# Kernel optimization log

Measured on AMD Instinct MI355X. Metric: run time of the kernel, lower is better.

Reference implementation:

```python
import jax, jax.numpy as jnp
import numpy as np

EPS = 1e-12  # matches torch F.normalize eps


def _l2_normalize(x):
    n = jnp.linalg.norm(x, axis=-1, keepdims=True)
    return x / jnp.maximum(n, EPS)


def setup_inputs() -> dict:
    key = jax.random.key(0)
    k1, k2, k3 = jax.random.split(key, 3)
    N, E, D = 100000, 1200000, 64
    feat = jax.random.normal(k1, (N, D), dtype=jnp.float32)
    beta = jnp.ones((1,), dtype=jnp.float32)
    src = jax.random.randint(k2, (E,), 0, N, dtype=jnp.int32)
    dst = jax.random.randint(k3, (E,), 0, N, dtype=jnp.int32)
    return {"feat": feat, "beta": beta, "src": src, "dst": dst}


def reference(feat, beta, src, dst):
    N = feat.shape[0]
    # cosine similarity on each edge (AGNN att_type)
    nh = _l2_normalize(feat)                                  # [N, D]
    e = beta[0] * jnp.sum(nh[src] * nh[dst], axis=-1)         # [E]
    # edge softmax over incoming edges of each destination node
    emax = jax.ops.segment_max(e, dst, num_segments=N)        # [N]
    emax = jnp.where(jnp.isfinite(emax), emax, 0.0)           # isolated nodes
    p = jnp.exp(e - emax[dst])                                # [E]
    psum = jax.ops.segment_sum(p, dst, num_segments=N)        # [N]
    p = p / jnp.maximum(psum[dst], EPS)                       # [E]
    # weighted scatter-sum aggregation: h_i' = sum_j p_ij * h_j
    msg = feat[src] * p[:, None]                              # [E, D]
    out = jax.ops.segment_sum(msg, dst, num_segments=N)       # [N, D]
    return out
```

## Files before the change

kernel.cpp:

```cpp
#include <hip/hip_runtime.h>
#include <hip/hip_fp16.h>

#define D 64
#define EPS 1e-12f
#define NPB 512
#define NPB_SHIFT 9
#define NB 256
#define CAP 8192
#define CAP_SHIFT 13
#define EPB 8192
#define SRC_BITS 17

typedef _Float16 hv2 __attribute__((ext_vector_type(2)));

__device__ inline unsigned bc_u(__half2 h) { return __builtin_bit_cast(unsigned, h); }
__device__ inline __half2  bc_h(unsigned u) { return __builtin_bit_cast(__half2, u); }

__device__ inline float fdot2f(unsigned a, unsigned b, float c) {
#if defined(__has_builtin) && __has_builtin(__builtin_amdgcn_fdot2)
    return __builtin_amdgcn_fdot2(__builtin_bit_cast(hv2, a),
                                  __builtin_bit_cast(hv2, b), c, false);
#else
    __half2 ah = bc_h(a), bh = bc_h(b);
    return c + __low2float(ah) * __low2float(bh)
             + __high2float(ah) * __high2float(bh);
#endif
}

__global__ __launch_bounds__(1024) void prep_scatter_kernel(
        const float4* __restrict__ feat4,
        float* __restrict__ norms,
        uint2* __restrict__ nh2,
        const int* __restrict__ src,
        const int* __restrict__ dst,
        int* __restrict__ bincursor,
        unsigned* __restrict__ pairs,
        int N, int E, int BI) {
    __shared__ int hist[NB], offs[NB], cursor[NB], gbase[NB], tmp[NB];
    __shared__ unsigned buf[EPB];
    __shared__ unsigned char binof[EPB];

    if ((int)blockIdx.x < BI) {
        int gid = blockIdx.x * 1024 + threadIdx.x;
        int row = gid >> 4;
        int lg  = gid & 15;
        if (row >= N) return;
        float4 v = feat4[row * 16 + lg];
        float ss = v.x * v.x + v.y * v.y + v.z * v.z + v.w * v.w;
        #pragma unroll
        for (int off = 1; off < 16; off <<= 1) ss += __shfl_xor(ss, off, 64);
        float nrm = fmaxf(sqrtf(ss), EPS);
        float inv = 1.0f / nrm;
        if (lg == 0) norms[row] = nrm;
        uint2 p;
        p.x = bc_u(__floats2half2_rn(v.x * inv, v.y * inv));
        p.y = bc_u(__floats2half2_rn(v.z * inv, v.w * inv));
        nh2[row * 16 + lg] = p;
        return;
    }

    int tid  = threadIdx.x;
    int base = (blockIdx.x - BI) * EPB;
    int cnt  = min(EPB, E - base);

    if (tid < NB) hist[tid] = 0;
    __syncthreads();
    for (int i = tid; i < cnt; i += 1024)
        atomicAdd(&hist[dst[base + i] >> NPB_SHIFT], 1);
    __syncthreads();
    int v = 0;
    if (tid < NB) { v = hist[tid]; tmp[tid] = v; }
    __syncthreads();
    #pragma unroll
    for (int off = 1; off < NB; off <<= 1) {
        int t = 0;
        if (tid < NB && tid >= off) t = tmp[tid - off];
        __syncthreads();
        if (tid < NB) tmp[tid] += t;
        __syncthreads();
    }
    if (tid < NB) {
        int e = tmp[tid] - v;
        offs[tid] = e; cursor[tid] = e;
        if (v > 0)
            gbase[tid] = (tid << CAP_SHIFT) + atomicAdd(&bincursor[tid], v);
    }
    __syncthreads();
    for (int i = tid; i < cnt; i += 1024) {
        int s = src[base + i], dd = dst[base + i];
        int b = dd >> NPB_SHIFT;
        int l = atomicAdd(&cursor[b], 1);
        buf[l]   = ((unsigned)(dd & (NPB - 1)) << SRC_BITS) | (unsigned)s;
        binof[l] = (unsigned char)b;
    }
    __syncthreads();
    for (int i = tid; i < cnt; i += 1024) {
        int b = binof[i];
        pairs[gbase[b] + (i - offs[b])] = buf[i];
    }
}

__global__ __launch_bounds__(1024) void csr_kernel(const unsigned* __restrict__ pairs,
                                                   const int* __restrict__ bincursor,
                                                   int* __restrict__ rowbeg,
                                                   int* __restrict__ rowend,
                                                   int* __restrict__ esrc, int N) {
    __shared__ unsigned buf[CAP];
    __shared__ int hist[NPB], cursor[NPB], tmp[NPB];
    int b    = blockIdx.x;
    int tid  = threadIdx.x;
    int base = b << CAP_SHIFT;
    int cnt  = bincursor[b];
    int node0 = b << NPB_SHIFT;

    if (tid < NPB) hist[tid] = 0;
    __syncthreads();
    for (int i = tid; i < cnt; i += 1024) {
        unsigned p = pairs[base + i];
        buf[i] = p;
        atomicAdd(&hist[p >> SRC_BITS], 1);
    }
    __syncthreads();
    int v = 0;
    if (tid < NPB) { v = hist[tid]; tmp[tid] = v; }
    __syncthreads();
    #pragma unroll
    for (int off = 1; off < NPB; off <<= 1) {
        int t = 0;
        if (tid < NPB && tid >= off) t = tmp[tid - off];
        __syncthreads();
        if (tid < NPB) tmp[tid] += t;
        __syncthreads();
    }
    if (tid < NPB) {
        int excl = tmp[tid] - v;
        cursor[tid] = excl;
        int node = node0 + tid;
        if (node < N) { rowbeg[node] = base + excl; rowend[node] = base + excl + v; }
    }
    __syncthreads();
    for (int i = tid; i < cnt; i += 1024) {
        unsigned p = buf[i];
        int pos = atomicAdd(&cursor[p >> SRC_BITS], 1);
        esrc[base + pos] = (int)(p & ((1u << SRC_BITS) - 1));
    }
}

__global__ __launch_bounds__(256) void gather_kernel(const uint4* __restrict__ nh4,
                                                     const float* __restrict__ norms,
                                                     const float* __restrict__ beta_p,
                                                     const int* __restrict__ rowbeg,
                                                     const int* __restrict__ rowend,
                                                     const int* __restrict__ esrc,
                                                     float4* __restrict__ out4, int N) {
    int gid  = blockIdx.x * blockDim.x + threadIdx.x;
    int d    = gid >> 6;
    int lane = threadIdx.x & 63;
    int g    = lane >> 3;
    int lg   = lane & 7;
    if (d >= N) return;

    int start = rowbeg[d];
    int end   = rowend[d];
    float beta = beta_p[0];

    uint4 fdp = nh4[(size_t)d * 8 + lg];

    __half2 acc0 = __float2half2_rn(0.f), acc1 = acc0, acc2 = acc0, acc3 = acc0;
    float ps = 0.f;

    for (int j0 = start; j0 < end; j0 += 16) {
        int  ja = j0 + g;
        int  jb = ja + 8;
        bool va = (ja < end), vb = (jb < end);
        int  sa = va ? esrc[ja] : 0;
        int  sb = vb ? esrc[jb] : 0;
        uint4 pa = nh4[(size_t)sa * 8 + lg];
        uint4 pb = nh4[(size_t)sb * 8 + lg];
        float nsa = norms[sa], nsb = norms[sb];
        float dpa = fdot2f(pa.x, fdp.x, 0.f);
        float dpb = fdot2f(pb.x, fdp.x, 0.f);
        dpa = fdot2f(pa.y, fdp.y, dpa);  dpb = fdot2f(pb.y, fdp.y, dpb);
        dpa = fdot2f(pa.z, fdp.z, dpa);  dpb = fdot2f(pb.z, fdp.z, dpb);
        dpa = fdot2f(pa.w, fdp.w, dpa);  dpb = fdot2f(pb.w, fdp.w, dpb);
        #pragma unroll
        for (int off = 1; off < 8; off <<= 1) {
            dpa += __shfl_xor(dpa, off, 64);
            dpb += __shfl_xor(dpb, off, 64);
        }
        float wa = va ? __expf(beta * dpa) : 0.f;
        float wb = vb ? __expf(beta * dpb) : 0.f;
        __half2 wa2 = __float2half2_rn(wa * nsa);
        __half2 wb2 = __float2half2_rn(wb * nsb);
        acc0 = __hfma2(wa2, bc_h(pa.x), acc0); acc0 = __hfma2(wb2, bc_h(pb.x), acc0);
        acc1 = __hfma2(wa2, bc_h(pa.y), acc1); acc1 = __hfma2(wb2, bc_h(pb.y), acc1);
        acc2 = __hfma2(wa2, bc_h(pa.z), acc2); acc2 = __hfma2(wb2, bc_h(pb.z), acc2);
        acc3 = __hfma2(wa2, bc_h(pa.w), acc3); acc3 = __hfma2(wb2, bc_h(pb.w), acc3);
        ps += wa + wb;
    }

    #pragma unroll
    for (int off = 8; off < 64; off <<= 1) {
        acc0 = __hadd2(acc0, bc_h(__shfl_xor(bc_u(acc0), off, 64)));
        acc1 = __hadd2(acc1, bc_h(__shfl_xor(bc_u(acc1), off, 64)));
        acc2 = __hadd2(acc2, bc_h(__shfl_xor(bc_u(acc2), off, 64)));
        acc3 = __hadd2(acc3, bc_h(__shfl_xor(bc_u(acc3), off, 64)));
        ps  += __shfl_xor(ps, off, 64);
    }

    if (g == 0) {
        float r = 1.0f / fmaxf(ps, EPS);
        float4 o0 = {__low2float(acc0) * r, __high2float(acc0) * r,
                     __low2float(acc1) * r, __high2float(acc1) * r};
        float4 o1 = {__low2float(acc2) * r, __high2float(acc2) * r,
                     __low2float(acc3) * r, __high2float(acc3) * r};
        out4[(size_t)d * 16 + lg * 2]     = o0;
        out4[(size_t)d * 16 + lg * 2 + 1] = o1;
    }
}

extern "C" void kernel_launch(void* const* d_in, const int* in_sizes, int n_in,
                              void* d_out, int out_size, void* d_ws, size_t ws_size,
                              hipStream_t stream) {
    const float* feat = (const float*)d_in[0];
    const float* beta = (const float*)d_in[1];
    const int*   src  = (const int*)d_in[2];
    const int*   dst  = (const int*)d_in[3];

    int N = in_sizes[0] / D;
    int E = in_sizes[2];
    int nbins = (N + NPB - 1) / NPB;

    unsigned* pairs     = (unsigned*)d_ws;
    int*      esrc      = (int*)(pairs + (size_t)nbins * CAP);
    unsigned* nhraw     = (unsigned*)(esrc + (size_t)nbins * CAP);
    float*    norms     = (float*)(nhraw + (size_t)N * 32);
    int*      bincursor = (int*)(norms + N);
    int*      rowbeg    = bincursor + NB;
    int*      rowend    = rowbeg + N;

    hipMemsetAsync(bincursor, 0, NB * sizeof(int), stream);

    int BI = (N * 16 + 1023) / 1024;
    int BS = (E + EPB - 1) / EPB;
    prep_scatter_kernel<<<BI + BS, 1024, 0, stream>>>(
        (const float4*)feat, norms, (uint2*)nhraw, src, dst, bincursor,
        pairs, N, E, BI);
    csr_kernel<<<nbins, 1024, 0, stream>>>(pairs, bincursor, rowbeg, rowend,
                                           esrc, N);
    gather_kernel<<<(N * 64 + 255) / 256, 256, 0, stream>>>(
        (const uint4*)nhraw, norms, beta, rowbeg, rowend, esrc,
        (float4*)d_out, N);
}
```

Baseline: 144.4 us.

## Map one destination node per 8-lane group in gather and cache dst in LDS

The gather kernel now gives each 8-lane group its own destination node instead of spreading one node across a whole 64-lane wavefront. That removes the cross-group shuffle reduction and the idle lanes on low-degree nodes, at the cost of divergence when node degrees differ within a wavefront. The scatter kernel also halves its edges per block and keeps dst values in shared memory, so the second pass does not reload them from global memory.

```diff
diff --git a/kernel.cpp b/kernel.cpp
--- a/kernel.cpp
+++ b/kernel.cpp
@@ -8,7 +8,7 @@
 #define NB 256
 #define CAP 8192
 #define CAP_SHIFT 13
-#define EPB 8192
+#define EPB 4096
 #define SRC_BITS 17
 
 typedef _Float16 hv2 __attribute__((ext_vector_type(2)));
@@ -37,6 +37,7 @@
         unsigned* __restrict__ pairs,
         int N, int E, int BI) {
     __shared__ int hist[NB], offs[NB], cursor[NB], gbase[NB], tmp[NB];
+    __shared__ int dstbuf[EPB];
     __shared__ unsigned buf[EPB];
     __shared__ unsigned char binof[EPB];
 
@@ -65,8 +66,11 @@
 
     if (tid < NB) hist[tid] = 0;
     __syncthreads();
-    for (int i = tid; i < cnt; i += 1024)
-        atomicAdd(&hist[dst[base + i] >> NPB_SHIFT], 1);
+    for (int i = tid; i < cnt; i += 1024) {
+        int dd = dst[base + i];
+        dstbuf[i] = dd;
+        atomicAdd(&hist[dd >> NPB_SHIFT], 1);
+    }
     __syncthreads();
     int v = 0;
     if (tid < NB) { v = hist[tid]; tmp[tid] = v; }
@@ -87,7 +91,7 @@
     }
     __syncthreads();
     for (int i = tid; i < cnt; i += 1024) {
-        int s = src[base + i], dd = dst[base + i];
+        int s = src[base + i], dd = dstbuf[i];
         int b = dd >> NPB_SHIFT;
         int l = atomicAdd(&cursor[b], 1);
         buf[l]   = ((unsigned)(dd & (NPB - 1)) << SRC_BITS) | (unsigned)s;
@@ -153,15 +157,15 @@
                                                      const int* __restrict__ rowend,
                                                      const int* __restrict__ esrc,
                                                      float4* __restrict__ out4, int N) {
-    int gid  = blockIdx.x * blockDim.x + threadIdx.x;
-    int d    = gid >> 6;
+    int t    = blockIdx.x * 256 + threadIdx.x;
     int lane = threadIdx.x & 63;
     int g    = lane >> 3;
     int lg   = lane & 7;
+    int d    = (t >> 6) * 8 + g;
     if (d >= N) return;
 
-    int start = rowbeg[d];
-    int end   = rowend[d];
+    int j   = rowbeg[d];
+    int end = rowend[d];
     float beta = beta_p[0];
 
     uint4 fdp = nh4[(size_t)d * 8 + lg];
@@ -169,12 +173,10 @@
     __half2 acc0 = __float2half2_rn(0.f), acc1 = acc0, acc2 = acc0, acc3 = acc0;
     float ps = 0.f;
 
-    for (int j0 = start; j0 < end; j0 += 16) {
-        int  ja = j0 + g;
-        int  jb = ja + 8;
-        bool va = (ja < end), vb = (jb < end);
-        int  sa = va ? esrc[ja] : 0;
-        int  sb = vb ? esrc[jb] : 0;
+    for (; j < end; j += 2) {
+        bool vb = (j + 1 < end);
+        int  sa = esrc[j];
+        int  sb = vb ? esrc[j + 1] : sa;
         uint4 pa = nh4[(size_t)sa * 8 + lg];
         uint4 pb = nh4[(size_t)sb * 8 + lg];
         float nsa = norms[sa], nsb = norms[sb];
@@ -188,7 +190,7 @@
             dpa += __shfl_xor(dpa, off, 64);
             dpb += __shfl_xor(dpb, off, 64);
         }
-        float wa = va ? __expf(beta * dpa) : 0.f;
+        float wa = __expf(beta * dpa);
         float wb = vb ? __expf(beta * dpb) : 0.f;
         __half2 wa2 = __float2half2_rn(wa * nsa);
         __half2 wb2 = __float2half2_rn(wb * nsb);
@@ -199,24 +201,13 @@
         ps += wa + wb;
     }
 
-    #pragma unroll
-    for (int off = 8; off < 64; off <<= 1) {
-        acc0 = __hadd2(acc0, bc_h(__shfl_xor(bc_u(acc0), off, 64)));
-        acc1 = __hadd2(acc1, bc_h(__shfl_xor(bc_u(acc1), off, 64)));
-        acc2 = __hadd2(acc2, bc_h(__shfl_xor(bc_u(acc2), off, 64)));
-        acc3 = __hadd2(acc3, bc_h(__shfl_xor(bc_u(acc3), off, 64)));
-        ps  += __shfl_xor(ps, off, 64);
-    }
-
-    if (g == 0) {
-        float r = 1.0f / fmaxf(ps, EPS);
-        float4 o0 = {__low2float(acc0) * r, __high2float(acc0) * r,
-                     __low2float(acc1) * r, __high2float(acc1) * r};
-        float4 o1 = {__low2float(acc2) * r, __high2float(acc2) * r,
-                     __low2float(acc3) * r, __high2float(acc3) * r};
-        out4[(size_t)d * 16 + lg * 2]     = o0;
-        out4[(size_t)d * 16 + lg * 2 + 1] = o1;
-    }
+    float r = 1.0f / fmaxf(ps, EPS);
+    float4 o0 = {__low2float(acc0) * r, __high2float(acc0) * r,
+                 __low2float(acc1) * r, __high2float(acc1) * r};
+    float4 o1 = {__low2float(acc2) * r, __high2float(acc2) * r,
+                 __low2float(acc3) * r, __high2float(acc3) * r};
+    out4[(size_t)d * 16 + lg * 2]     = o0;
+    out4[(size_t)d * 16 + lg * 2 + 1] = o1;
 }
 
 extern "C" void kernel_launch(void* const* d_in, const int* in_sizes, int n_in,
@@ -248,7 +239,7 @@
         pairs, N, E, BI);
     csr_kernel<<<nbins, 1024, 0, stream>>>(pairs, bincursor, rowbeg, rowend,
                                            esrc, N);
-    gather_kernel<<<(N * 64 + 255) / 256, 256, 0, stream>>>(
+    gather_kernel<<<(N + 31) / 32, 256, 0, stream>>>(
         (const uint4*)nhraw, norms, beta, rowbeg, rowend, esrc,
         (float4*)d_out, N);
 }
```

Measured after the change: 140.7 us. 1.03x faster.
